# Performance work log

Hardware: AMD Instinct MI355X
Metric: run time of the kernel (lower is better)

Reference implementation:

```python
import jax, jax.numpy as jnp
import numpy as np

NLAYERS, NHEAD, ATTN_LEN, DMODEL, DHID, NTOKEN = 9, 2, 5, 128, 512, 2
HD = DMODEL // NHEAD
B, T, F = 4, 4096, 128
INV_SQRT_HD = 1.0 / float(np.sqrt(HD))


def setup_inputs() -> dict:
    key = jax.random.key(0)
    ks = iter(jax.random.split(key, 64))
    def w(shape, s=0.02):
        return jax.random.normal(next(ks), shape, jnp.float32) * s
    return dict(
        x=jax.random.normal(next(ks), (B, T, F), jnp.float32),
        conv1_w=w((32, 1, 5, 3)), conv1_b=jnp.zeros((32,), jnp.float32),
        conv2_w=w((64, 32, 1, 12)), conv2_b=jnp.zeros((64,), jnp.float32),
        conv3_w=w((DMODEL, 64, 3, 6)), conv3_b=jnp.zeros((DMODEL,), jnp.float32),
        ln1_s=jnp.ones((NLAYERS, DMODEL), jnp.float32), ln1_b=jnp.zeros((NLAYERS, DMODEL), jnp.float32),
        ln2_s=jnp.ones((NLAYERS, DMODEL), jnp.float32), ln2_b=jnp.zeros((NLAYERS, DMODEL), jnp.float32),
        Wq=w((NLAYERS, DMODEL, DMODEL)), bq=jnp.zeros((NLAYERS, DMODEL), jnp.float32),
        Wk=w((NLAYERS, DMODEL, DMODEL)), bk=jnp.zeros((NLAYERS, DMODEL), jnp.float32),
        Wv=w((NLAYERS, DMODEL, DMODEL)), bv=jnp.zeros((NLAYERS, DMODEL), jnp.float32),
        Wo=w((NLAYERS, DMODEL, DMODEL)), bo=jnp.zeros((NLAYERS, DMODEL), jnp.float32),
        Er=w((NLAYERS, NHEAD, ATTN_LEN, HD)),
        W1=w((NLAYERS, DMODEL, DHID)), b1=jnp.zeros((NLAYERS, DHID), jnp.float32),
        W2=w((NLAYERS, DHID, DMODEL)), b2=jnp.zeros((NLAYERS, DMODEL), jnp.float32),
        Wout=w((DMODEL, NTOKEN)), bout=jnp.zeros((NTOKEN,), jnp.float32),
        Wt=w((DMODEL, 300)), bt=jnp.zeros((300,), jnp.float32),
    )


def _ln(x, s, b, eps=1e-5):
    m = x.mean(-1, keepdims=True)
    v = ((x - m) ** 2).mean(-1, keepdims=True)
    return (x - m) * jax.lax.rsqrt(v + eps) * s + b


def _conv(x, w, b, pad_h):
    y = jax.lax.conv_general_dilated(x, w, (1, 1), ((pad_h, pad_h), (0, 0)),
                                     dimension_numbers=('NCHW', 'OIHW', 'NCHW'))
    return y + b[None, :, None, None]


def _pool3(x):
    # MaxPool2d(kernel=(1,3), stride=(1,3)) on freq axis
    return jax.lax.reduce_window(x, -jnp.inf, jax.lax.max, (1, 1, 1, 3), (1, 1, 1, 3), 'VALID')


def _attn(x, Wq, bq, Wk, bk, Wv, bv, Wo, bo, Er, layer):
    # Dilated windowed attention: query t attends to t + (k - attn_len//2)*2^layer
    Bb, Tt, D = x.shape
    dil = 2 ** layer
    c = ATTN_LEN // 2
    q = (x @ Wq + bq).reshape(Bb, Tt, NHEAD, HD)
    k = (x @ Wk + bk).reshape(Bb, Tt, NHEAD, HD)
    v = (x @ Wv + bv).reshape(Bb, Tt, NHEAD, HD)
    offs = (jnp.arange(Tt)[:, None] + (jnp.arange(ATTN_LEN) - c)[None, :] * dil)  # (T, a)
    valid = (offs >= 0) & (offs < Tt)
    idx = jnp.clip(offs, 0, Tt - 1)
    kg = k[:, idx]  # (B, T, a, H, hd)
    vg = v[:, idx]
    scores = (jnp.einsum('bthd,btahd->bhta', q, kg)
              + jnp.einsum('bthd,had->bhta', q, Er)) * INV_SQRT_HD
    scores = jnp.where(valid[None, None], scores, -jnp.inf)
    a = jax.nn.softmax(scores, axis=-1)
    out = jnp.einsum('bhta,btahd->bthd', a, vg).reshape(Bb, Tt, D)
    return out @ Wo + bo


def _forward(x, conv1_w, conv1_b, conv2_w, conv2_b, conv3_w, conv3_b,
             ln1_s, ln1_b, ln2_s, ln2_b, Wq, bq, Wk, bk, Wv, bv, Wo, bo, Er,
             W1, b1, W2, b2, Wout, bout, Wt, bt):
    h = x[:, None]                                    # (B,1,T,F)
    h = jax.nn.relu(_pool3(_conv(h, conv1_w, conv1_b, 2)))
    h = jax.nn.relu(_pool3(_conv(h, conv2_w, conv2_b, 0)))
    h = jax.nn.relu(_pool3(_conv(h, conv3_w, conv3_b, 1)))  # (B,D,T,1)
    h = h[:, :, :, 0].transpose(0, 2, 1)              # (B,T,D)
    skips = []
    for l in range(NLAYERS):
        skip = _attn(_ln(h, ln1_s[l], ln1_b[l]), Wq[l], bq[l], Wk[l], bk[l],
                     Wv[l], bv[l], Wo[l], bo[l], Er[l], l)
        h = h + skip
        z = _ln(h, ln2_s[l], ln2_b[l])
        h = h + jax.nn.relu(z @ W1[l] + b1[l]) @ W2[l] + b2[l]
        skips.append(skip)
    out = jax.nn.relu(h) @ Wout + bout                # (B,T,ntoken)
    t = jax.nn.relu(sum(skips)).mean(axis=1) @ Wt + bt  # (B,300)
    return out, t


def reference(x, conv1_w, conv1_b, conv2_w, conv2_b, conv3_w, conv3_b,
              ln1_s, ln1_b, ln2_s, ln2_b, Wq, bq, Wk, bk, Wv, bv, Wo, bo, Er,
              W1, b1, W2, b2, Wout, bout, Wt, bt):
    return _forward(x, conv1_w, conv1_b, conv2_w, conv2_b, conv3_w, conv3_b,
                    ln1_s, ln1_b, ln2_s, ln2_b, Wq, bq, Wk, bk, Wv, bv, Wo, bo, Er,
                    W1, b1, W2, b2, Wout, bout, Wt, bt)
```

## Files before the change

kernel.cpp:

```cpp
#include <hip/hip_runtime.h>

#define T_ 4096
#define B_ 4

typedef unsigned short u16;
typedef __bf16 bf16x8 __attribute__((ext_vector_type(8)));
typedef float f32x4 __attribute__((ext_vector_type(4)));

__device__ inline void splitbf(float v, u16& h, u16& l) {
  __bf16 hb = (__bf16)v;
  float r = v - (float)hb;
  __bf16 lb = (__bf16)r;
  h = __builtin_bit_cast(u16, hb);
  l = __builtin_bit_cast(u16, lb);
}

#define MFMA(a,b,c) __builtin_amdgcn_mfma_f32_16x16x32_bf16((a),(b),(c),0,0,0)

__global__ __launch_bounds__(256) void k_conv12m(
    const float* __restrict__ x, const float* __restrict__ w1,
    const float* __restrict__ b1,
    const u16* __restrict__ wh, const u16* __restrict__ wl,
    const float* __restrict__ b2,
    u16* __restrict__ oh, u16* __restrict__ ol)
{
  __shared__ float sx[12][130];
  __shared__ float w1s[480];
  __shared__ float b1s[32];
  __shared__ u16 sh[8*43*40];
  __shared__ u16 sl[8*43*40];
  __shared__ float dmp[4][15][66];
  const int tid = threadIdx.x;
  const int t0 = blockIdx.x * 8;
  const int b = blockIdx.y;
  const float* xb = x + (size_t)b*T_*128;
  for (int i = tid; i < 1536; i += 256) {
    int r = i >> 7, c = i & 127;
    int t = t0 - 2 + r;
    sx[r][c] = (t >= 0 && t < T_) ? xb[t*128 + c] : 0.f;
  }
  for (int i = tid; i < 480; i += 256) w1s[i] = w1[i];
  if (tid < 32) b1s[tid] = b1[tid];
  for (int i = tid; i < 320; i += 256) {
    int tt = i / 40, c = i - tt*40;
    sh[(tt*43 + 42)*40 + c] = 0;
    sl[(tt*43 + 42)*40 + c] = 0;
  }
  __syncthreads();
  for (int i = tid; i < 10752; i += 256) {
    int c1 = i & 31;
    int wp = (i >> 5) % 42;
    int tt = i / 1344;
    float m = -1e30f;
    #pragma unroll
    for (int j = 0; j < 3; j++) {
      float acc = 0.f;
      int wb = wp*3 + j;
      #pragma unroll
      for (int kh = 0; kh < 5; kh++)
        #pragma unroll
        for (int kw = 0; kw < 3; kw++)
          acc += sx[tt+kh][wb+kw] * w1s[c1*15 + kh*3 + kw];
      m = fmaxf(m, acc);
    }
    float v = fmaxf(m + b1s[c1], 0.f);
    u16 hh, ll; splitbf(v, hh, ll);
    int dd = (tt*43 + wp)*40 + c1;
    sh[dd] = hh; sl[dd] = ll;
  }
  __syncthreads();
  const int lane = tid & 63;
  const int wid = tid >> 6;
  const int lr = lane & 15;
  const int lk8 = (lane >> 4) * 8;
  f32x4 acc[2][2][4] = {};
  #pragma unroll 3
  for (int kw = 0; kw < 12; kw++) {
    bf16x8 bh[4], bl[4];
    #pragma unroll
    for (int nf = 0; nf < 4; nf++) {
      int go = ((nf*12 + kw) << 9) + (lane << 3);
      bh[nf] = *(const bf16x8*)(wh + go);
      bl[nf] = *(const bf16x8*)(wl + go);
    }
    #pragma unroll
    for (int tp = 0; tp < 2; tp++) {
      int tloc = wid*2 + tp;
      #pragma unroll
      for (int mf = 0; mf < 2; mf++) {
        int lofs = (tloc*43 + mf*16 + lr + kw)*40 + lk8;
        bf16x8 ah = *(const bf16x8*)&sh[lofs];
        bf16x8 al = *(const bf16x8*)&sl[lofs];
        #pragma unroll
        for (int nf = 0; nf < 4; nf++) {
          acc[tp][mf][nf] = MFMA(ah, bl[nf], acc[tp][mf][nf]);
          acc[tp][mf][nf] = MFMA(al, bh[nf], acc[tp][mf][nf]);
          acc[tp][mf][nf] = MFMA(ah, bh[nf], acc[tp][mf][nf]);
        }
      }
    }
  }
  const int lg = lane >> 4;
  for (int tp = 0; tp < 2; tp++) {
    int t = t0 + wid*2 + tp;
    for (int half = 0; half < 2; half++) {
      #pragma unroll
      for (int mf = 0; mf < 2; mf++)
        #pragma unroll
        for (int r = 0; r < 4; r++) {
          int grow = mf*16 + lg*4 + r;
          int lrow = grow - half*15;
          if (lrow >= 0 && lrow < 15) {
            #pragma unroll
            for (int nf = 0; nf < 4; nf++)
              dmp[wid][lrow][nf*16 + lr] = acc[tp][mf][nf][r];
          }
        }
      asm volatile("s_waitcnt lgkmcnt(0)" ::: "memory");
      #pragma unroll
      for (int it = 0; it < 5; it++) {
        float v = fmaxf(fmaxf(dmp[wid][it*3][lane], dmp[wid][it*3+1][lane]),
                        dmp[wid][it*3+2][lane]);
        v = fmaxf(v + b2[lane], 0.f);
        u16 hh, ll; splitbf(v, hh, ll);
        size_t o = (size_t)((b*T_ + t)*10 + half*5 + it)*64 + lane;
        oh[o] = hh; ol[o] = ll;
      }
      asm volatile("s_waitcnt lgkmcnt(0)" ::: "memory");
    }
  }
}

__global__ __launch_bounds__(256) void k_conv3m(
    const u16* __restrict__ ih, const u16* __restrict__ il,
    const u16* __restrict__ wh, const u16* __restrict__ wl,
    const float* __restrict__ b3, float* __restrict__ hout)
{
  __shared__ u16 sh[18*720];
  __shared__ u16 sl[18*720];
  __shared__ float dmp[48][132];
  const int tid = threadIdx.x;
  const int t0 = (blockIdx.x & 255) * 16;
  const int b = blockIdx.y;
  for (int i = tid; i < 1440; i += 256) {
    int cg = i & 7;
    int w = (i >> 3) % 10;
    int tt = i / 80;
    int t = t0 - 1 + tt;
    int dd = tt*720 + w*72 + cg*8;
    if (t >= 0 && t < T_) {
      size_t so = (size_t)((b*T_ + t)*10 + w)*64 + cg*8;
      *(ulonglong2*)&sh[dd] = *(const ulonglong2*)&ih[so];
      *(ulonglong2*)&sl[dd] = *(const ulonglong2*)&il[so];
    } else {
      ulonglong2 z; z.x = 0; z.y = 0;
      *(ulonglong2*)&sh[dd] = z;
      *(ulonglong2*)&sl[dd] = z;
    }
  }
  __syncthreads();
  const int lane = tid & 63;
  const int wid = tid >> 6;
  const int lr = lane & 15;
  const int lk8 = (lane >> 4) * 8;
  int tlm[3], wom[3];
  #pragma unroll
  for (int mf = 0; mf < 3; mf++) {
    int r = mf*16 + lr;
    tlm[mf] = r / 3;
    wom[mf] = r - tlm[mf]*3;
  }
  f32x4 acc[3][2] = {};
  #pragma unroll 2
  for (int kh = 0; kh < 3; kh++) {
    #pragma unroll
    for (int kw = 0; kw < 6; kw++) {
      #pragma unroll
      for (int chh = 0; chh < 2; chh++) {
        int s = (kh*6 + kw)*2 + chh;
        int ch = chh*32;
        bf16x8 bh[2], bl[2];
        #pragma unroll
        for (int nfl = 0; nfl < 2; nfl++) {
          int go = (((wid*2 + nfl)*36 + s) << 9) + (lane << 3);
          bh[nfl] = *(const bf16x8*)(wh + go);
          bl[nfl] = *(const bf16x8*)(wl + go);
        }
        #pragma unroll
        for (int mf = 0; mf < 3; mf++) {
          int lofs = (tlm[mf] + kh)*720 + (wom[mf] + kw)*72 + ch + lk8;
          bf16x8 ah = *(const bf16x8*)&sh[lofs];
          bf16x8 al = *(const bf16x8*)&sl[lofs];
          #pragma unroll
          for (int nfl = 0; nfl < 2; nfl++) {
            acc[mf][nfl] = MFMA(ah, bl[nfl], acc[mf][nfl]);
            acc[mf][nfl] = MFMA(al, bh[nfl], acc[mf][nfl]);
            acc[mf][nfl] = MFMA(ah, bh[nfl], acc[mf][nfl]);
          }
        }
      }
    }
  }
  const int lg = lane >> 4;
  #pragma unroll
  for (int mf = 0; mf < 3; mf++)
    #pragma unroll
    for (int r = 0; r < 4; r++) {
      int row = mf*16 + lg*4 + r;
      #pragma unroll
      for (int nfl = 0; nfl < 2; nfl++)
        dmp[row][wid*32 + nfl*16 + lr] = acc[mf][nfl][r];
    }
  __syncthreads();
  for (int i = tid; i < 2048; i += 256) {
    int c3 = i & 127;
    int tt = i >> 7;
    float v = fmaxf(fmaxf(dmp[tt*3][c3], dmp[tt*3+1][c3]), dmp[tt*3+2][c3]);
    v = fmaxf(v + b3[c3], 0.f);
    hout[(size_t)(b*T_ + t0 + tt)*128 + c3] = v;
  }
}

__device__ inline float wave_sum(float v) {
  #pragma unroll
  for (int m = 1; m < 64; m <<= 1) v += __shfl_xor(v, m, 64);
  return v;
}

__global__ __launch_bounds__(256) void k_ln(
    const float* __restrict__ in, const float* __restrict__ sc,
    const float* __restrict__ bi, u16* __restrict__ oh, u16* __restrict__ ol)
{
  const int lane = threadIdx.x & 63;
  const int row = blockIdx.x*4 + (threadIdx.x >> 6);
  float a = in[row*128 + lane];
  float c = in[row*128 + 64 + lane];
  float mean = wave_sum(a + c) * (1.f/128.f);
  float d0 = a - mean, d1 = c - mean;
  float var = wave_sum(d0*d0 + d1*d1) * (1.f/128.f);
  float rs = rsqrtf(var + 1e-5f);
  float v0 = d0*rs*sc[lane]    + bi[lane];
  float v1 = d1*rs*sc[64+lane] + bi[64+lane];
  u16 h0, l0, h1, l1;
  splitbf(v0, h0, l0); splitbf(v1, h1, l1);
  oh[row*128 + lane] = h0;      ol[row*128 + lane] = l0;
  oh[row*128 + 64 + lane] = h1; ol[row*128 + 64 + lane] = l1;
}

__device__ inline void prep_fr(const float* __restrict__ src,
                               u16* __restrict__ dh, u16* __restrict__ dl,
                               int K, int N, int matStride, int idx)
{
  int mat = idx / (K*N);
  int rem = idx - mat*(K*N);
  int k = rem / N;
  int n = rem - k*N;
  float v = src[idx];
  u16 h, l; splitbf(v, h, l);
  int nt = n >> 4, ks = k >> 5, ksub = k & 31;
  size_t o = (size_t)mat*matStride + (size_t)((nt*(K>>5) + ks) << 9)
           + (((ksub >> 3) << 4) + (n & 15))*8 + (ksub & 7);
  dh[o] = h; dl[o] = l;
}

__global__ __launch_bounds__(256) void k_wprep_all(
    const float* __restrict__ Wq, const float* __restrict__ Wk,
    const float* __restrict__ Wv, const float* __restrict__ Wo,
    const float* __restrict__ W1, const float* __restrict__ W2,
    const float* __restrict__ c2w, const float* __restrict__ c3w,
    u16* wqkv_h, u16* wqkv_l, u16* wo_h, u16* wo_l,
    u16* w1t_h, u16* w1t_l, u16* w2t_h, u16* w2t_l,
    u16* wc2_h, u16* wc2_l, u16* wc3_h, u16* wc3_l)
{
  const int bid = blockIdx.x;
  const int tid = threadIdx.x;
  if (bid < 576) {
    prep_fr(Wq, wqkv_h, wqkv_l, 128, 128, 49152, bid*256 + tid);
  } else if (bid < 1152) {
    prep_fr(Wk, wqkv_h + 16384, wqkv_l + 16384, 128, 128, 49152, (bid-576)*256 + tid);
  } else if (bid < 1728) {
    prep_fr(Wv, wqkv_h + 32768, wqkv_l + 32768, 128, 128, 49152, (bid-1152)*256 + tid);
  } else if (bid < 2304) {
    prep_fr(Wo, wo_h, wo_l, 128, 128, 16384, (bid-1728)*256 + tid);
  } else if (bid < 4608) {
    prep_fr(W1, w1t_h, w1t_l, 128, 512, 65536, (bid-2304)*256 + tid);
  } else if (bid < 6912) {
    prep_fr(W2, w2t_h, w2t_l, 512, 128, 65536, (bid-4608)*256 + tid);
  } else if (bid < 7008) {
    int idx = (bid-6912)*256 + tid;
    int c2 = idx / 384;
    int rem = idx - c2*384;
    int c1 = rem / 12;
    int kw = rem - c1*12;
    float v = c2w[idx];
    u16 h, l; splitbf(v, h, l);
    size_t o = (size_t)((((c2 >> 4)*12 + kw) << 9))
             + (((c1 >> 3) << 4) + (c2 & 15))*8 + (c1 & 7);
    wc2_h[o] = h; wc2_l[o] = l;
  } else {
    int idx = (bid-7008)*256 + tid;
    int c3 = idx / 1152;
    int rem = idx - c3*1152;
    int c2 = rem / 18;
    int khkw = rem - c2*18;
    float v = c3w[idx];
    u16 h, l; splitbf(v, h, l);
    int s = khkw*2 + (c2 >> 5);
    int c = c2 & 31;
    size_t o = (size_t)((((c3 >> 4)*36 + s) << 9))
             + (((c >> 3) << 4) + (c3 & 15))*8 + (c & 7);
    wc3_h[o] = h; wc3_l[o] = l;
  }
}

__global__ __launch_bounds__(256) void k_gqkv(
    const u16* __restrict__ Ah, const u16* __restrict__ Al,
    const u16* __restrict__ Wh, const u16* __restrict__ Wl,
    const float* __restrict__ bq, const float* __restrict__ bk,
    const float* __restrict__ bv, float* __restrict__ outbase)
{
  __shared__ u16 sAh[16*136], sAl[16*136];
  const int tid = threadIdx.x;
  const int m0 = blockIdx.x * 16;
  const int z = blockIdx.y;
  const u16* wh = Wh + z*16384;
  const u16* wl = Wl + z*16384;
  const float* bias = (z == 0) ? bq : (z == 1) ? bk : bv;
  float* C = outbase + (size_t)z*2097152;
  {
    int row = tid >> 4, c8 = tid & 15;
    *(ulonglong2*)&sAh[row*136 + c8*8] = *(const ulonglong2*)&Ah[(size_t)(m0+row)*128 + c8*8];
    *(ulonglong2*)&sAl[row*136 + c8*8] = *(const ulonglong2*)&Al[(size_t)(m0+row)*128 + c8*8];
  }
  __syncthreads();
  const int lane = tid & 63, nq = tid >> 6;
  const int lr = lane & 15, lg = lane >> 4, l8 = lg*8;
  f32x4 acc[2] = {};
  #pragma unroll
  for (int ks = 0; ks < 4; ks++) {
    bf16x8 ah = *(const bf16x8*)&sAh[lr*136 + ks*32 + l8];
    bf16x8 al = *(const bf16x8*)&sAl[lr*136 + ks*32 + l8];
    #pragma unroll
    for (int nf = 0; nf < 2; nf++) {
      int go = (((nq*2 + nf)*4 + ks) << 9) + (lane << 3);
      bf16x8 bh = *(const bf16x8*)(wh + go);
      bf16x8 bl = *(const bf16x8*)(wl + go);
      acc[nf] = MFMA(ah, bl, acc[nf]);
      acc[nf] = MFMA(al, bh, acc[nf]);
      acc[nf] = MFMA(ah, bh, acc[nf]);
    }
  }
  #pragma unroll
  for (int nf = 0; nf < 2; nf++) {
    int col = nq*32 + nf*16 + lr;
    float bb = bias[col];
    #pragma unroll
    for (int r = 0; r < 4; r++)
      C[(size_t)(m0 + lg*4 + r)*128 + col] = acc[nf][r] + bb;
  }
}

__global__ __launch_bounds__(512) void k_attnwo(
    const float* __restrict__ qb, const float* __restrict__ kb,
    const float* __restrict__ vb, const float* __restrict__ Er,
    const u16* __restrict__ Wh, const u16* __restrict__ Wl,
    const float* __restrict__ bo, const float* __restrict__ sc,
    const float* __restrict__ bi,
    float* __restrict__ hbuf, float* __restrict__ ssum, int skip_init,
    u16* __restrict__ oh, u16* __restrict__ ol, int dil)
{
  __shared__ u16 sAh[32*136], sAl[32*136];
  __shared__ float dmp[32*132];
  const int tid = threadIdx.x, lane = tid & 63, wv = tid >> 6;
  const int m0 = blockIdx.x * 32;
  const int b = m0 >> 12;
  const int t0 = m0 & 4095;
  for (int rr = 0; rr < 4; rr++) {
    int r = wv*4 + rr;
    int t = t0 + r;
    int bt = m0 + r;
    #pragma unroll
    for (int h = 0; h < 2; h++) {
      float qd = qb[(size_t)bt*128 + h*64 + lane];
      float s[5];
      int tpc_arr[5];
      #pragma unroll
      for (int a = 0; a < 5; a++) {
        int tp = t + (a-2)*dil;
        bool valid = (tp >= 0 && tp < T_);
        int tpc = tp < 0 ? 0 : (tp > T_-1 ? T_-1 : tp);
        tpc_arr[a] = tpc;
        float kd = kb[(size_t)(b*T_ + tpc)*128 + h*64 + lane];
        float er = Er[(h*5 + a)*64 + lane];
        float p = qd * (kd + er);
        p = wave_sum(p);
        s[a] = valid ? p * 0.125f : -1e30f;
      }
      float mx = s[0];
      #pragma unroll
      for (int a = 1; a < 5; a++) mx = fmaxf(mx, s[a]);
      float p[5], psum = 0.f;
      #pragma unroll
      for (int a = 0; a < 5; a++) { p[a] = __expf(s[a]-mx); psum += p[a]; }
      float inv = 1.f/psum;
      float o = 0.f;
      #pragma unroll
      for (int a = 0; a < 5; a++)
        o += p[a] * vb[(size_t)(b*T_ + tpc_arr[a])*128 + h*64 + lane];
      float vo = o * inv;
      u16 hh, ll; splitbf(vo, hh, ll);
      sAh[r*136 + h*64 + lane] = hh;
      sAl[r*136 + h*64 + lane] = ll;
    }
  }
  __syncthreads();
  const int lr = lane & 15, lg = lane >> 4, l8 = lg*8;
  const int mq = wv >> 2, nq = wv & 3;
  f32x4 acc[2] = {};
  #pragma unroll
  for (int ks = 0; ks < 4; ks++) {
    bf16x8 ah = *(const bf16x8*)&sAh[(mq*16 + lr)*136 + ks*32 + l8];
    bf16x8 al = *(const bf16x8*)&sAl[(mq*16 + lr)*136 + ks*32 + l8];
    #pragma unroll
    for (int nf = 0; nf < 2; nf++) {
      int go = (((nq*2 + nf)*4 + ks) << 9) + (lane << 3);
      bf16x8 bh = *(const bf16x8*)(Wh + go);
      bf16x8 bl = *(const bf16x8*)(Wl + go);
      acc[nf] = MFMA(ah, bl, acc[nf]);
      acc[nf] = MFMA(al, bh, acc[nf]);
      acc[nf] = MFMA(ah, bh, acc[nf]);
    }
  }
  #pragma unroll
  for (int nf = 0; nf < 2; nf++) {
    int col = nq*32 + nf*16 + lr;
    float bb = bo[col];
    #pragma unroll
    for (int r = 0; r < 4; r++) {
      int row = mq*16 + lg*4 + r;
      size_t o = (size_t)(m0 + row)*128 + col;
      float val = acc[nf][r] + bb;
      if (skip_init) ssum[o] = val; else ssum[o] += val;
      float hn = hbuf[o] + val;
      hbuf[o] = hn;
      dmp[row*132 + col] = hn;
    }
  }
  __syncthreads();
  const int row = tid >> 4, p = tid & 15;
  float xv[8], s = 0.f;
  const float* dp = &dmp[row*132 + p*8];
  #pragma unroll
  for (int i = 0; i < 8; i++) { xv[i] = dp[i]; s += xv[i]; }
  s += __shfl_xor(s, 1); s += __shfl_xor(s, 2);
  s += __shfl_xor(s, 4); s += __shfl_xor(s, 8);
  float mean = s * (1.f/128.f);
  float v = 0.f;
  #pragma unroll
  for (int i = 0; i < 8; i++) { float d = xv[i]-mean; v += d*d; }
  v += __shfl_xor(v, 1); v += __shfl_xor(v, 2);
  v += __shfl_xor(v, 4); v += __shfl_xor(v, 8);
  float rs = rsqrtf(v*(1.f/128.f) + 1e-5f);
  size_t gro = (size_t)(m0 + row)*128;
  #pragma unroll
  for (int i = 0; i < 8; i++) {
    int c = p*8 + i;
    float y = (xv[i]-mean)*rs*sc[c] + bi[c];
    u16 hh, ll; splitbf(y, hh, ll);
    oh[gro + c] = hh; ol[gro + c] = ll;
  }
}

__global__ __launch_bounds__(512) void k_ffnqkv(
    const u16* __restrict__ Ah, const u16* __restrict__ Al,
    const u16* __restrict__ W1h, const u16* __restrict__ W1l,
    const float* __restrict__ b1,
    const u16* __restrict__ W2h, const u16* __restrict__ W2l,
    const float* __restrict__ b2,
    float* __restrict__ hbuf, int do_qkv,
    const float* __restrict__ sc, const float* __restrict__ bi,
    const u16* __restrict__ Qh, const u16* __restrict__ Ql,
    const float* __restrict__ bq, const float* __restrict__ bk,
    const float* __restrict__ bv, float* __restrict__ qkvout)
{
  __shared__ u16 sAh[32*136], sAl[32*136];
  __shared__ u16 hidH[2][32*136], hidL[2][32*136];
  __shared__ float dmp[32*132];
  const int tid = threadIdx.x, lane = tid & 63;
  const int m0 = blockIdx.x * 32;
  {
    int row = tid >> 4, c8 = tid & 15;
    *(ulonglong2*)&sAh[row*136 + c8*8] = *(const ulonglong2*)&Ah[(size_t)(m0+row)*128 + c8*8];
    *(ulonglong2*)&sAl[row*136 + c8*8] = *(const ulonglong2*)&Al[(size_t)(m0+row)*128 + c8*8];
  }
  __syncthreads();
  const int wv = tid >> 6, mq = wv >> 2, nq = wv & 3;
  const int lr = lane & 15, lg = lane >> 4, l8 = lg*8;
  f32x4 acc2[2] = {};
  for (int c = 0; c < 4; c++) {
    f32x4 acc1[2] = {};
    #pragma unroll
    for (int ks = 0; ks < 4; ks++) {
      bf16x8 ah = *(const bf16x8*)&sAh[(mq*16 + lr)*136 + ks*32 + l8];
      bf16x8 al = *(const bf16x8*)&sAl[(mq*16 + lr)*136 + ks*32 + l8];
      #pragma unroll
      for (int nf = 0; nf < 2; nf++) {
        int go = (((c*8 + nq*2 + nf)*4 + ks) << 9) + (lane << 3);
        bf16x8 bh = *(const bf16x8*)(W1h + go);
        bf16x8 bl = *(const bf16x8*)(W1l + go);
        acc1[nf] = MFMA(ah, bl, acc1[nf]);
        acc1[nf] = MFMA(al, bh, acc1[nf]);
        acc1[nf] = MFMA(ah, bh, acc1[nf]);
      }
    }
    __syncthreads();
    #pragma unroll
    for (int nf = 0; nf < 2; nf++) {
      int col = nq*32 + nf*16 + lr;
      float bb = b1[c*128 + col];
      #pragma unroll
      for (int r = 0; r < 4; r++) {
        int row = mq*16 + lg*4 + r;
        float hv = fmaxf(acc1[nf][r] + bb, 0.f);
        u16 hh, ll; splitbf(hv, hh, ll);
        hidH[c & 1][row*136 + col] = hh;
        hidL[c & 1][row*136 + col] = ll;
      }
    }
    __syncthreads();
    #pragma unroll
    for (int ks = 0; ks < 4; ks++) {
      bf16x8 ah = *(const bf16x8*)&hidH[c & 1][(mq*16 + lr)*136 + ks*32 + l8];
      bf16x8 al = *(const bf16x8*)&hidL[c & 1][(mq*16 + lr)*136 + ks*32 + l8];
      #pragma unroll
      for (int nf = 0; nf < 2; nf++) {
        int go = (((nq*2 + nf)*16 + c*4 + ks) << 9) + (lane << 3);
        bf16x8 bh = *(const bf16x8*)(W2h + go);
        bf16x8 bl = *(const bf16x8*)(W2l + go);
        acc2[nf] = MFMA(ah, bl, acc2[nf]);
        acc2[nf] = MFMA(al, bh, acc2[nf]);
        acc2[nf] = MFMA(ah, bh, acc2[nf]);
      }
    }
  }
  #pragma unroll
  for (int nf = 0; nf < 2; nf++) {
    int col = nq*32 + nf*16 + lr;
    float bb = b2[col];
    #pragma unroll
    for (int r = 0; r < 4; r++) {
      int row = mq*16 + lg*4 + r;
      size_t o = (size_t)(m0 + row)*128 + col;
      float hn = hbuf[o] + acc2[nf][r] + bb;
      hbuf[o] = hn;
      dmp[row*132 + col] = hn;
    }
  }
  if (!do_qkv) return;
  __syncthreads();
  {
    const int row = tid >> 4, p = tid & 15;
    float xv[8], s = 0.f;
    const float* dp = &dmp[row*132 + p*8];
    #pragma unroll
    for (int i = 0; i < 8; i++) { xv[i] = dp[i]; s += xv[i]; }
    s += __shfl_xor(s, 1); s += __shfl_xor(s, 2);
    s += __shfl_xor(s, 4); s += __shfl_xor(s, 8);
    float mean = s * (1.f/128.f);
    float v = 0.f;
    #pragma unroll
    for (int i = 0; i < 8; i++) { float d = xv[i]-mean; v += d*d; }
    v += __shfl_xor(v, 1); v += __shfl_xor(v, 2);
    v += __shfl_xor(v, 4); v += __shfl_xor(v, 8);
    float rs = rsqrtf(v*(1.f/128.f) + 1e-5f);
    #pragma unroll
    for (int i = 0; i < 8; i++) {
      int cc = p*8 + i;
      float y = (xv[i]-mean)*rs*sc[cc] + bi[cc];
      u16 hh, ll; splitbf(y, hh, ll);
      sAh[row*136 + cc] = hh; sAl[row*136 + cc] = ll;
    }
  }
  __syncthreads();
  for (int z = 0; z < 3; z++) {
    const u16* wh = Qh + z*16384;
    const u16* wl = Ql + z*16384;
    const float* bias = (z == 0) ? bq : (z == 1) ? bk : bv;
    float* C = qkvout + (size_t)z*2097152;
    f32x4 acc[2] = {};
    #pragma unroll
    for (int ks = 0; ks < 4; ks++) {
      bf16x8 ah = *(const bf16x8*)&sAh[(mq*16 + lr)*136 + ks*32 + l8];
      bf16x8 al = *(const bf16x8*)&sAl[(mq*16 + lr)*136 + ks*32 + l8];
      #pragma unroll
      for (int nf = 0; nf < 2; nf++) {
        int go = (((nq*2 + nf)*4 + ks) << 9) + (lane << 3);
        bf16x8 bh = *(const bf16x8*)(wh + go);
        bf16x8 bl = *(const bf16x8*)(wl + go);
        acc[nf] = MFMA(ah, bl, acc[nf]);
        acc[nf] = MFMA(al, bh, acc[nf]);
        acc[nf] = MFMA(ah, bh, acc[nf]);
      }
    }
    #pragma unroll
    for (int nf = 0; nf < 2; nf++) {
      int col = nq*32 + nf*16 + lr;
      float bb = bias[col];
      #pragma unroll
      for (int r = 0; r < 4; r++)
        C[(size_t)(m0 + mq*16 + lg*4 + r)*128 + col] = acc[nf][r] + bb;
    }
  }
}

__global__ __launch_bounds__(256) void k_out(
    const float* __restrict__ h, const float* __restrict__ Wout,
    const float* __restrict__ bout, float* __restrict__ out)
{
  int idx = blockIdx.x*256 + threadIdx.x;
  int bt = idx >> 1, j = idx & 1;
  float acc = bout[j];
  const float* hp = &h[bt*128];
  #pragma unroll 4
  for (int k2 = 0; k2 < 128; k2++)
    acc += fmaxf(hp[k2], 0.f) * Wout[k2*2 + j];
  out[idx] = acc;
}

__global__ __launch_bounds__(256) void k_red1(
    const float* __restrict__ ss, float* __restrict__ part)
{
  __shared__ float red[256];
  int b = blockIdx.x >> 5, g = blockIdx.x & 31;
  int c = threadIdx.x & 127, hf = threadIdx.x >> 7;
  float acc = 0.f;
  for (int i2 = 0; i2 < 64; i2++) {
    int t = g*128 + i2*2 + hf;
    acc += fmaxf(ss[(b*T_ + t)*128 + c], 0.f);
  }
  red[threadIdx.x] = acc;
  __syncthreads();
  if (threadIdx.x < 128)
    part[(b*32+g)*128 + threadIdx.x] = red[threadIdx.x] + red[threadIdx.x+128];
}

__global__ __launch_bounds__(512) void k_tail2(
    const float* __restrict__ part, const float* __restrict__ Wt,
    const float* __restrict__ btb, float* __restrict__ out)
{
  __shared__ float mb[512];
  const int tid = threadIdx.x;
  int b = tid >> 7, c = tid & 127;
  float s = 0.f;
  for (int g = 0; g < 32; g++) s += part[(b*32+g)*128 + c];
  mb[tid] = s * (1.f/4096.f);
  __syncthreads();
  for (int i = tid; i < 1200; i += 512) {
    int bb = i / 300, j = i - bb*300;
    float acc = btb[j];
    #pragma unroll 4
    for (int k2 = 0; k2 < 128; k2++)
      acc += mb[bb*128 + k2] * Wt[k2*300 + j];
    out[32768 + i] = acc;
  }
}

extern "C" void kernel_launch(void* const* d_in, const int* in_sizes, int n_in,
                              void* d_out, int out_size, void* d_ws, size_t ws_size,
                              hipStream_t stream)
{
  const float* x    = (const float*)d_in[0];
  const float* c1w  = (const float*)d_in[1];
  const float* c1b  = (const float*)d_in[2];
  const float* c2w  = (const float*)d_in[3];
  const float* c2b  = (const float*)d_in[4];
  const float* c3w  = (const float*)d_in[5];
  const float* c3b  = (const float*)d_in[6];
  const float* ln1s = (const float*)d_in[7];
  const float* ln1b = (const float*)d_in[8];
  const float* ln2s = (const float*)d_in[9];
  const float* ln2b = (const float*)d_in[10];
  const float* Wq   = (const float*)d_in[11];
  const float* bq   = (const float*)d_in[12];
  const float* Wk   = (const float*)d_in[13];
  const float* bk   = (const float*)d_in[14];
  const float* Wv   = (const float*)d_in[15];
  const float* bv   = (const float*)d_in[16];
  const float* Wo   = (const float*)d_in[17];
  const float* bo   = (const float*)d_in[18];
  const float* Er   = (const float*)d_in[19];
  const float* W1   = (const float*)d_in[20];
  const float* b1   = (const float*)d_in[21];
  const float* W2   = (const float*)d_in[22];
  const float* b2   = (const float*)d_in[23];
  const float* Wout = (const float*)d_in[24];
  const float* bout = (const float*)d_in[25];
  const float* Wt   = (const float*)d_in[26];
  const float* bt   = (const float*)d_in[27];

  char* W = (char*)d_ws;
  u16* c2o_h = (u16*)W;
  u16* c2o_l = (u16*)(W + 20971520);
  char* RB = W + 33554432;
  float* qb  = (float*)RB;
  float* kb  = qb + 2097152;
  float* vb2 = qb + 4194304;
  u16* xh    = (u16*)(RB + 25165824);
  u16* xlo   = (u16*)(RB + 29360128);
  char* RC = W + 67108864;
  float* hbuf = (float*)RC;
  float* ssum = (float*)(RC + 8388608);
  u16* wqkv_h = (u16*)(RC + 16777216);
  u16* wqkv_l = wqkv_h + 442368;
  u16* wo_h   = wqkv_l + 442368;
  u16* wo_l   = wo_h + 147456;
  u16* w1t_h  = wo_l + 147456;
  u16* w1t_l  = w1t_h + 589824;
  u16* w2t_h  = w1t_l + 589824;
  u16* w2t_l  = w2t_h + 589824;
  u16* wc2_h  = w2t_l + 589824;
  u16* wc2_l  = wc2_h + 24576;
  u16* wc3_h  = wc2_l + 24576;
  u16* wc3_l  = wc3_h + 147456;
  float* part  = (float*)(wc3_l + 147456);
  float* outf  = (float*)d_out;

  k_wprep_all<<<7584, 256, 0, stream>>>(
      Wq, Wk, Wv, Wo, W1, W2, c2w, c3w,
      wqkv_h, wqkv_l, wo_h, wo_l, w1t_h, w1t_l, w2t_h, w2t_l,
      wc2_h, wc2_l, wc3_h, wc3_l);

  k_conv12m<<<dim3(512, B_), 256, 0, stream>>>(x, c1w, c1b, wc2_h, wc2_l, c2b,
                                               c2o_h, c2o_l);
  k_conv3m<<<dim3(256, B_), 256, 0, stream>>>(c2o_h, c2o_l, wc3_h, wc3_l, c3b, hbuf);

  k_ln<<<4096, 256, 0, stream>>>(hbuf, ln1s, ln1b, xh, xlo);
  k_gqkv<<<dim3(1024, 3), 256, 0, stream>>>(
      xh, xlo, wqkv_h, wqkv_l, bq, bk, bv, qb);

  for (int l = 0; l < 9; l++) {
    int ln = (l < 8) ? (l + 1) : 0;
    k_attnwo<<<512, 512, 0, stream>>>(
        qb, kb, vb2, Er + l*640,
        wo_h + l*16384, wo_l + l*16384, bo + l*128,
        ln2s + l*128, ln2b + l*128,
        hbuf, ssum, (l == 0) ? 1 : 0, xh, xlo, 1 << l);
    k_ffnqkv<<<512, 512, 0, stream>>>(
        xh, xlo, w1t_h + l*65536, w1t_l + l*65536, b1 + l*512,
        w2t_h + l*65536, w2t_l + l*65536, b2 + l*128,
        hbuf, (l < 8) ? 1 : 0,
        ln1s + ln*128, ln1b + ln*128,
        wqkv_h + ln*49152, wqkv_l + ln*49152,
        bq + ln*128, bk + ln*128, bv + ln*128, qb);
  }

  k_out<<<128, 256, 0, stream>>>(hbuf, Wout, bout, outf);
  k_red1<<<128, 256, 0, stream>>>(ssum, part);
  k_tail2<<<1, 512, 0, stream>>>(part, Wt, bt, outf);
}
```

Before: 712.6 us.

## Fuse attention+Wo with FFN+QKV into one per-layer kernel, double-buffer QKV

Merges the per-layer attention/output-projection kernel and the FFN/next-QKV kernel into a single kernel. The LN2 output now stays in shared memory instead of going through global bf16 hi/lo buffers, and one launch per layer is removed. QKV outputs are ping-ponged between two buffers so that blocks reading neighbouring rows' K/V are not overwritten by other blocks writing next-layer QKV. The conv1 stage is also restructured so each thread keeps its filter in registers and reuses overlapping input columns across the three pooled positions. The merged kernel uses more shared memory, which may lower occupancy.

```diff
diff --git a/kernel.cpp b/kernel.cpp
--- a/kernel.cpp
+++ b/kernel.cpp
@@ -47,26 +47,30 @@
     sl[(tt*43 + 42)*40 + c] = 0;
   }
   __syncthreads();
-  for (int i = tid; i < 10752; i += 256) {
-    int c1 = i & 31;
-    int wp = (i >> 5) % 42;
-    int tt = i / 1344;
-    float m = -1e30f;
-    #pragma unroll
-    for (int j = 0; j < 3; j++) {
-      float acc = 0.f;
-      int wb = wp*3 + j;
-      #pragma unroll
-      for (int kh = 0; kh < 5; kh++)
-        #pragma unroll
-        for (int kw = 0; kw < 3; kw++)
-          acc += sx[tt+kh][wb+kw] * w1s[c1*15 + kh*3 + kw];
-      m = fmaxf(m, acc);
-    }
-    float v = fmaxf(m + b1s[c1], 0.f);
-    u16 hh, ll; splitbf(v, hh, ll);
-    int dd = (tt*43 + wp)*40 + c1;
-    sh[dd] = hh; sl[dd] = ll;
+  {
+    const int c1 = tid & 31, tt = tid >> 5;
+    float w1r[15];
+    #pragma unroll
+    for (int i = 0; i < 15; i++) w1r[i] = w1s[c1*15 + i];
+    float bb1 = b1s[c1];
+    for (int wp = 0; wp < 42; wp++) {
+      int c0 = wp*3;
+      float s0 = 0.f, s1 = 0.f, s2 = 0.f;
+      #pragma unroll
+      for (int kh = 0; kh < 5; kh++) {
+        float x0 = sx[tt+kh][c0],   x1 = sx[tt+kh][c0+1];
+        float x2 = sx[tt+kh][c0+2], x3 = sx[tt+kh][c0+3];
+        float x4 = sx[tt+kh][c0+4];
+        float wA = w1r[kh*3], wB = w1r[kh*3+1], wC = w1r[kh*3+2];
+        s0 += x0*wA + x1*wB + x2*wC;
+        s1 += x1*wA + x2*wB + x3*wC;
+        s2 += x2*wA + x3*wB + x4*wC;
+      }
+      float v = fmaxf(fmaxf(fmaxf(s0, s1), s2) + bb1, 0.f);
+      u16 hh, ll; splitbf(v, hh, ll);
+      int dd = (tt*43 + wp)*40 + c1;
+      sh[dd] = hh; sl[dd] = ll;
+    }
   }
   __syncthreads();
   const int lane = tid & 63;
@@ -360,21 +364,33 @@
   }
 }
 
-__global__ __launch_bounds__(512) void k_attnwo(
-    const float* __restrict__ qb, const float* __restrict__ kb,
-    const float* __restrict__ vb, const float* __restrict__ Er,
-    const u16* __restrict__ Wh, const u16* __restrict__ Wl,
-    const float* __restrict__ bo, const float* __restrict__ sc,
-    const float* __restrict__ bi,
+__global__ __launch_bounds__(512) void k_layer(
+    const float* __restrict__ qin,
+    const float* __restrict__ Er,
+    const u16* __restrict__ Woh, const u16* __restrict__ Wol,
+    const float* __restrict__ bo,
+    const float* __restrict__ sc2, const float* __restrict__ bi2,
+    const u16* __restrict__ W1h, const u16* __restrict__ W1l,
+    const float* __restrict__ b1,
+    const u16* __restrict__ W2h, const u16* __restrict__ W2l,
+    const float* __restrict__ b2,
     float* __restrict__ hbuf, float* __restrict__ ssum, int skip_init,
-    u16* __restrict__ oh, u16* __restrict__ ol, int dil)
+    int do_qkv,
+    const float* __restrict__ sc1, const float* __restrict__ bi1,
+    const u16* __restrict__ Qh, const u16* __restrict__ Ql,
+    const float* __restrict__ bq, const float* __restrict__ bk,
+    const float* __restrict__ bv, float* __restrict__ qout, int dil)
 {
   __shared__ u16 sAh[32*136], sAl[32*136];
+  __shared__ u16 hidH[2][32*136], hidL[2][32*136];
   __shared__ float dmp[32*132];
   const int tid = threadIdx.x, lane = tid & 63, wv = tid >> 6;
   const int m0 = blockIdx.x * 32;
   const int b = m0 >> 12;
   const int t0 = m0 & 4095;
+  const float* qb = qin;
+  const float* kb = qin + 2097152;
+  const float* vb = qin + 4194304;
   for (int rr = 0; rr < 4; rr++) {
     int r = wv*4 + rr;
     int t = t0 + r;
@@ -416,86 +432,63 @@
   __syncthreads();
   const int lr = lane & 15, lg = lane >> 4, l8 = lg*8;
   const int mq = wv >> 2, nq = wv & 3;
-  f32x4 acc[2] = {};
-  #pragma unroll
-  for (int ks = 0; ks < 4; ks++) {
-    bf16x8 ah = *(const bf16x8*)&sAh[(mq*16 + lr)*136 + ks*32 + l8];
-    bf16x8 al = *(const bf16x8*)&sAl[(mq*16 + lr)*136 + ks*32 + l8];
+  {
+    f32x4 acc[2] = {};
+    #pragma unroll
+    for (int ks = 0; ks < 4; ks++) {
+      bf16x8 ah = *(const bf16x8*)&sAh[(mq*16 + lr)*136 + ks*32 + l8];
+      bf16x8 al = *(const bf16x8*)&sAl[(mq*16 + lr)*136 + ks*32 + l8];
+      #pragma unroll
+      for (int nf = 0; nf < 2; nf++) {
+        int go = (((nq*2 + nf)*4 + ks) << 9) + (lane << 3);
+        bf16x8 bh = *(const bf16x8*)(Woh + go);
+        bf16x8 bl = *(const bf16x8*)(Wol + go);
+        acc[nf] = MFMA(ah, bl, acc[nf]);
+        acc[nf] = MFMA(al, bh, acc[nf]);
+        acc[nf] = MFMA(ah, bh, acc[nf]);
+      }
+    }
     #pragma unroll
     for (int nf = 0; nf < 2; nf++) {
-      int go = (((nq*2 + nf)*4 + ks) << 9) + (lane << 3);
-      bf16x8 bh = *(const bf16x8*)(Wh + go);
-      bf16x8 bl = *(const bf16x8*)(Wl + go);
-      acc[nf] = MFMA(ah, bl, acc[nf]);
-      acc[nf] = MFMA(al, bh, acc[nf]);
-      acc[nf] = MFMA(ah, bh, acc[nf]);
-    }
-  }
-  #pragma unroll
-  for (int nf = 0; nf < 2; nf++) {
-    int col = nq*32 + nf*16 + lr;
-    float bb = bo[col];
-    #pragma unroll
-    for (int r = 0; r < 4; r++) {
-      int row = mq*16 + lg*4 + r;
-      size_t o = (size_t)(m0 + row)*128 + col;
-      float val = acc[nf][r] + bb;
-      if (skip_init) ssum[o] = val; else ssum[o] += val;
-      float hn = hbuf[o] + val;
-      hbuf[o] = hn;
-      dmp[row*132 + col] = hn;
-    }
-  }
-  __syncthreads();
-  const int row = tid >> 4, p = tid & 15;
-  float xv[8], s = 0.f;
-  const float* dp = &dmp[row*132 + p*8];
-  #pragma unroll
-  for (int i = 0; i < 8; i++) { xv[i] = dp[i]; s += xv[i]; }
-  s += __shfl_xor(s, 1); s += __shfl_xor(s, 2);
-  s += __shfl_xor(s, 4); s += __shfl_xor(s, 8);
-  float mean = s * (1.f/128.f);
-  float v = 0.f;
-  #pragma unroll
-  for (int i = 0; i < 8; i++) { float d = xv[i]-mean; v += d*d; }
-  v += __shfl_xor(v, 1); v += __shfl_xor(v, 2);
-  v += __shfl_xor(v, 4); v += __shfl_xor(v, 8);
-  float rs = rsqrtf(v*(1.f/128.f) + 1e-5f);
-  size_t gro = (size_t)(m0 + row)*128;
-  #pragma unroll
-  for (int i = 0; i < 8; i++) {
-    int c = p*8 + i;
-    float y = (xv[i]-mean)*rs*sc[c] + bi[c];
-    u16 hh, ll; splitbf(y, hh, ll);
-    oh[gro + c] = hh; ol[gro + c] = ll;
-  }
-}
-
-__global__ __launch_bounds__(512) void k_ffnqkv(
-    const u16* __restrict__ Ah, const u16* __restrict__ Al,
-    const u16* __restrict__ W1h, const u16* __restrict__ W1l,
-    const float* __restrict__ b1,
-    const u16* __restrict__ W2h, const u16* __restrict__ W2l,
-    const float* __restrict__ b2,
-    float* __restrict__ hbuf, int do_qkv,
-    const float* __restrict__ sc, const float* __restrict__ bi,
-    const u16* __restrict__ Qh, const u16* __restrict__ Ql,
-    const float* __restrict__ bq, const float* __restrict__ bk,
-    const float* __restrict__ bv, float* __restrict__ qkvout)
-{
-  __shared__ u16 sAh[32*136], sAl[32*136];
-  __shared__ u16 hidH[2][32*136], hidL[2][32*136];
-  __shared__ float dmp[32*132];
-  const int tid = threadIdx.x, lane = tid & 63;
-  const int m0 = blockIdx.x * 32;
+      int col = nq*32 + nf*16 + lr;
+      float bb = bo[col];
+      #pragma unroll
+      for (int r = 0; r < 4; r++) {
+        int row = mq*16 + lg*4 + r;
+        size_t o = (size_t)(m0 + row)*128 + col;
+        float val = acc[nf][r] + bb;
+        if (skip_init) ssum[o] = val; else ssum[o] += val;
+        float hn = hbuf[o] + val;
+        hbuf[o] = hn;
+        dmp[row*132 + col] = hn;
+      }
+    }
+  }
+  __syncthreads();
   {
-    int row = tid >> 4, c8 = tid & 15;
-    *(ulonglong2*)&sAh[row*136 + c8*8] = *(const ulonglong2*)&Ah[(size_t)(m0+row)*128 + c8*8];
-    *(ulonglong2*)&sAl[row*136 + c8*8] = *(const ulonglong2*)&Al[(size_t)(m0+row)*128 + c8*8];
-  }
-  __syncthreads();
-  const int wv = tid >> 6, mq = wv >> 2, nq = wv & 3;
-  const int lr = lane & 15, lg = lane >> 4, l8 = lg*8;
+    const int row = tid >> 4, p = tid & 15;
+    float xv[8], s = 0.f;
+    const float* dp = &dmp[row*132 + p*8];
+    #pragma unroll
+    for (int i = 0; i < 8; i++) { xv[i] = dp[i]; s += xv[i]; }
+    s += __shfl_xor(s, 1); s += __shfl_xor(s, 2);
+    s += __shfl_xor(s, 4); s += __shfl_xor(s, 8);
+    float mean = s * (1.f/128.f);
+    float v = 0.f;
+    #pragma unroll
+    for (int i = 0; i < 8; i++) { float d = xv[i]-mean; v += d*d; }
+    v += __shfl_xor(v, 1); v += __shfl_xor(v, 2);
+    v += __shfl_xor(v, 4); v += __shfl_xor(v, 8);
+    float rs = rsqrtf(v*(1.f/128.f) + 1e-5f);
+    #pragma unroll
+    for (int i = 0; i < 8; i++) {
+      int cc = p*8 + i;
+      float y = (xv[i]-mean)*rs*sc2[cc] + bi2[cc];
+      u16 hh, ll; splitbf(y, hh, ll);
+      sAh[row*136 + cc] = hh; sAl[row*136 + cc] = ll;
+    }
+  }
+  __syncthreads();
   f32x4 acc2[2] = {};
   for (int c = 0; c < 4; c++) {
     f32x4 acc1[2] = {};
@@ -576,7 +569,7 @@
     #pragma unroll
     for (int i = 0; i < 8; i++) {
       int cc = p*8 + i;
-      float y = (xv[i]-mean)*rs*sc[cc] + bi[cc];
+      float y = (xv[i]-mean)*rs*sc1[cc] + bi1[cc];
       u16 hh, ll; splitbf(y, hh, ll);
       sAh[row*136 + cc] = hh; sAl[row*136 + cc] = ll;
     }
@@ -586,7 +579,7 @@
     const u16* wh = Qh + z*16384;
     const u16* wl = Ql + z*16384;
     const float* bias = (z == 0) ? bq : (z == 1) ? bk : bv;
-    float* C = qkvout + (size_t)z*2097152;
+    float* C = qout + (size_t)z*2097152;
     f32x4 acc[2] = {};
     #pragma unroll
     for (int ks = 0; ks < 4; ks++) {
@@ -701,13 +694,12 @@
   char* W = (char*)d_ws;
   u16* c2o_h = (u16*)W;
   u16* c2o_l = (u16*)(W + 20971520);
-  char* RB = W + 33554432;
-  float* qb  = (float*)RB;
-  float* kb  = qb + 2097152;
-  float* vb2 = qb + 4194304;
-  u16* xh    = (u16*)(RB + 25165824);
-  u16* xlo   = (u16*)(RB + 29360128);
-  char* RC = W + 67108864;
+  char* RB = W + 41943040;
+  float* qbuf0 = (float*)RB;
+  float* qbuf1 = (float*)(RB + 25165824);
+  u16* xh    = (u16*)(RB + 50331648);
+  u16* xlo   = (u16*)(RB + 54525952);
+  char* RC = W + 100663296;
   float* hbuf = (float*)RC;
   float* ssum = (float*)(RC + 8388608);
   u16* wqkv_h = (u16*)(RC + 16777216);
@@ -717,6 +709,7 @@
   u16* w1t_h  = wo_l + 147456;
   u16* w1t_l  = w1t_h + 589824;
   u16* w2t_h  = w1t_l + 589824;
+  u16* w2t_h2 = w2t_h;  (void)w2t_h2;
   u16* w2t_l  = w2t_h + 589824;
   u16* wc2_h  = w2t_l + 589824;
   u16* wc2_l  = wc2_h + 24576;
@@ -736,22 +729,23 @@
 
   k_ln<<<4096, 256, 0, stream>>>(hbuf, ln1s, ln1b, xh, xlo);
   k_gqkv<<<dim3(1024, 3), 256, 0, stream>>>(
-      xh, xlo, wqkv_h, wqkv_l, bq, bk, bv, qb);
+      xh, xlo, wqkv_h, wqkv_l, bq, bk, bv, qbuf0);
 
   for (int l = 0; l < 9; l++) {
     int ln = (l < 8) ? (l + 1) : 0;
-    k_attnwo<<<512, 512, 0, stream>>>(
-        qb, kb, vb2, Er + l*640,
+    float* qin  = (l & 1) ? qbuf1 : qbuf0;
+    float* qout = (l & 1) ? qbuf0 : qbuf1;
+    k_layer<<<512, 512, 0, stream>>>(
+        qin, Er + l*640,
         wo_h + l*16384, wo_l + l*16384, bo + l*128,
         ln2s + l*128, ln2b + l*128,
-        hbuf, ssum, (l == 0) ? 1 : 0, xh, xlo, 1 << l);
-    k_ffnqkv<<<512, 512, 0, stream>>>(
-        xh, xlo, w1t_h + l*65536, w1t_l + l*65536, b1 + l*512,
+        w1t_h + l*65536, w1t_l + l*65536, b1 + l*512,
         w2t_h + l*65536, w2t_l + l*65536, b2 + l*128,
-        hbuf, (l < 8) ? 1 : 0,
+        hbuf, ssum, (l == 0) ? 1 : 0,
+        (l < 8) ? 1 : 0,
         ln1s + ln*128, ln1b + ln*128,
         wqkv_h + ln*49152, wqkv_l + ln*49152,
-        bq + ln*128, bk + ln*128, bv + ln*128, qb);
+        bq + ln*128, bk + ln*128, bv + ln*128, qout, 1 << l);
   }
 
   k_out<<<128, 256, 0, stream>>>(hbuf, Wout, bout, outf);
```

New measurement: 671.5 us. 1.06x faster.
